# Kernel optimization log

Measured on AMD Instinct MI355X. Metric: run time of the kernel, lower is better.

The kernel has to match this reference:

```python
import jax, jax.numpy as jnp
from jax import lax
import numpy as np

B, N, E, U = 128, 1024, 300, 128
L = 512          # num_leaves per sample
NN = 2 * L - 1   # num_nodes per sample (binary tree)


def _hsig(x):
    # Keras hard_sigmoid: clip(0.2*x + 0.5, 0, 1)
    return jnp.clip(0.2 * x + 0.5, 0.0, 1.0)


def setup_inputs() -> dict:
    key = jax.random.key(0)
    ks = jax.random.split(key, 5)
    rng = np.random.default_rng(0)
    # children of node t are uniform in [0, t) -> valid bottom-up binary tree
    u = rng.random((B, N, 2))
    child = (u * np.arange(N)[None, :, None]).astype(np.int32)
    child[:, :L, :] = 0  # leaves have no children (never read)
    num_vecs = np.tile(np.array([[NN, L]], np.int32), (B, 1))
    return {
        "initial_state": jax.random.normal(ks[0], (B, N, E), jnp.float32),
        "translation_kernel": jax.random.normal(ks[1], (E, U), jnp.float32) * 0.05,
        "kernel": jax.random.normal(ks[2], (5 * U, U), jnp.float32) * 0.05,
        "recurrent_kernel": jax.random.normal(ks[3], (5 * U, 2 * U), jnp.float32) * 0.05,
        "bias": jnp.zeros((5 * U, 1), jnp.float32),
        "child_vecs": jnp.asarray(child),
        "num_vecs": jnp.asarray(num_vecs),
    }


def reference(initial_state, translation_kernel, kernel, recurrent_kernel, bias,
              child_vecs, num_vecs):
    b, n, _ = initial_state.shape
    units = kernel.shape[1]
    # leaf initial states: relu(x @ W_translate)  -> [B, N, U]
    x = jax.nn.relu(jnp.einsum('bne,eu->bnu', initial_state, translation_kernel))
    num_nodes = num_vecs[:, 0]
    num_leaves = num_vecs[:, 1]
    bvec = bias[:, 0][None, :]  # [1, 5U]

    def step(carry, t):
        H, C = carry  # [B, N, U] each
        ch = jnp.take(child_vecs, t, axis=1)                                   # [B, 2]
        h_ch = jnp.take_along_axis(H, ch[:, :, None], axis=1).reshape(b, 2 * units)
        c_ch = jnp.take_along_axis(C, ch[:, :, None], axis=1).reshape(b, 2 * units)
        xt = jnp.take(x, t, axis=1)                                            # [B, U]
        # z = kernel @ x^T + recurrent_kernel @ [h_l; h_r] + bias  (batched, [B, 5U])
        z = xt @ kernel.T + h_ch @ recurrent_kernel.T + bvec
        i = _hsig(z[:, :units])
        f = _hsig(z[:, units:3 * units])                                       # [B, 2U]
        o = _hsig(z[:, 3 * units:4 * units])
        g = jnp.tanh(z[:, 4 * units:])
        # faithful to original: reshape (flat_mem*f) as [U, 2] row-major, sum axis 1
        c_new = (c_ch * f).reshape(b, units, 2).sum(axis=-1) + i * g
        h_new = o * jnp.tanh(c_new)
        act = ((t >= num_leaves) & (t < num_nodes))[:, None]                   # [B, 1]
        h_upd = jnp.where(act, h_new, jnp.take(H, t, axis=1))
        c_upd = jnp.where(act, c_new, jnp.take(C, t, axis=1))
        H = lax.dynamic_update_slice(H, h_upd[:, None, :], (0, t, 0))
        C = lax.dynamic_update_slice(C, c_upd[:, None, :], (0, t, 0))
        return (H, C), None

    # leaves start with hidden = memory = translated vec; internal nodes overwritten in order
    (H, _), _ = lax.scan(step, (x, x), jnp.arange(n))
    valid = (jnp.arange(n)[None, :] < num_nodes[:, None])[..., None]
    return H * valid.astype(H.dtype)
```

## Files before the change

kernel.cpp:

```cpp
#include <hip/hip_runtime.h>
#include <hip/hip_bf16.h>

#define B_ 128
#define N_ 1024
#define E_ 300
#define U_ 128
#define M_ (B_ * N_)
#define Z_ (5 * U_)
#define LMAXT 40
#define LPAR 20

typedef __attribute__((ext_vector_type(8))) short bf16x8;
typedef __attribute__((ext_vector_type(4))) float f32x4;
typedef _Float16 f16x4 __attribute__((ext_vector_type(4)));
typedef _Float16 f16x8 __attribute__((ext_vector_type(8)));

__device__ __forceinline__ short f2bf(float f) {
  unsigned u = __builtin_bit_cast(unsigned, f);
  u = (u + 0x7fffu + ((u >> 16) & 1u)) >> 16;
  return (short)u;
}

__device__ __forceinline__ float hsig(float z) {
  float v = __builtin_fmaf(z, 0.2f, 0.5f);
  v = v < 0.f ? 0.f : v;
  v = v > 1.f ? 1.f : v;
  return v;
}

__device__ __forceinline__ float tanh_fast(float x) {
  float p = __expf(2.f * x);
  return 1.f - 2.f * __builtin_amdgcn_rcpf(p + 1.f);
}

__device__ __forceinline__ unsigned pk2(float a, float b) {
  return __builtin_bit_cast(unsigned, __builtin_amdgcn_cvt_pkrtz(a, b));
}

__device__ __forceinline__ f16x8 pack8(float4 a, float4 b) {
  uint4 u;
  u.x = pk2(a.x, a.y);
  u.y = pk2(a.z, a.w);
  u.z = pk2(b.x, b.y);
  u.w = pk2(b.z, b.w);
  return __builtin_bit_cast(f16x8, u);
}

__global__ __launch_bounds__(256) void prep(
    const float* __restrict__ Wr, const float* __restrict__ Wk,
    _Float16* __restrict__ W16, _Float16* __restrict__ Wk16) {
  const int idx = blockIdx.x * 256 + threadIdx.x;
  if (idx < 163840) {
    W16[idx] = (_Float16)Wr[idx];
  } else if (idx < 245760) {
    const int i = idx - 163840;
    Wk16[i] = (_Float16)Wk[i];
  }
}

__global__ __launch_bounds__(256) void x_gemm(
    const float* __restrict__ A, const float* __restrict__ W,
    float* __restrict__ H) {
  __shared__ __align__(16) short As[64][40];
  __shared__ __align__(16) short Ws[128][40];
  const int tid = threadIdx.x;
  const int m0 = blockIdx.x * 64;
  f32x4 acc[8] = {};
  const int lane = tid & 63, wv = tid >> 6;
  const int lr = lane & 15, lg = lane >> 4;

  for (int kc = 0; kc < 10; ++kc) {
    const int k0 = kc * 32;
    {
      const int row = tid >> 2, kk = (tid & 3) * 8;
      const float* src = A + (size_t)(m0 + row) * E_ + k0 + kk;
      bf16x8 v;
      if (k0 + 32 <= E_) {
#pragma unroll
        for (int i = 0; i < 8; ++i) v[i] = f2bf(src[i]);
      } else {
#pragma unroll
        for (int i = 0; i < 8; ++i)
          v[i] = (k0 + kk + i < E_) ? f2bf(src[i]) : (short)0;
      }
      *(bf16x8*)&As[row][kk] = v;
    }
#pragma unroll
    for (int s = 0; s < 2; ++s) {
      const int slot = tid + s * 256;
      const int n = slot & 127, kg = slot >> 7;
      bf16x8 v;
      if (k0 + 32 <= E_) {
#pragma unroll
        for (int i = 0; i < 8; ++i) v[i] = f2bf(W[(k0 + kg * 8 + i) * U_ + n]);
      } else {
#pragma unroll
        for (int i = 0; i < 8; ++i) {
          const int k = k0 + kg * 8 + i;
          v[i] = (k < E_) ? f2bf(W[k * U_ + n]) : (short)0;
        }
      }
      *(bf16x8*)&Ws[n][kg * 8] = v;
    }
    __syncthreads();
    bf16x8 a = *(const bf16x8*)&As[wv * 16 + lr][lg * 8];
#pragma unroll
    for (int nt = 0; nt < 8; ++nt) {
      bf16x8 b = *(const bf16x8*)&Ws[nt * 16 + lr][lg * 8];
      acc[nt] = __builtin_amdgcn_mfma_f32_16x16x32_bf16(a, b, acc[nt], 0, 0, 0);
    }
    __syncthreads();
  }
#pragma unroll
  for (int nt = 0; nt < 8; ++nt) {
#pragma unroll
    for (int r = 0; r < 4; ++r) {
      const int m = m0 + wv * 16 + lg * 4 + r;
      const int n = nt * 16 + lr;
      float v = acc[nt][r];
      v = v > 0.f ? v : 0.f;
      H[(size_t)m * U_ + n] = v;
    }
  }
}

__global__ __launch_bounds__(256) void xz_gemm(
    const float* __restrict__ X, const _Float16* __restrict__ Wk16,
    const float* __restrict__ bias, const int* __restrict__ nv,
    _Float16* __restrict__ XZ) {
  const int m0 = blockIdx.x * 64;
  {
    const int bb = m0 >> 10;
    const int t0 = m0 & (N_ - 1);
    const int nodes = nv[2 * bb], leaves = nv[2 * bb + 1];
    if (t0 + 64 <= leaves || t0 >= nodes) return;
  }
  __shared__ __align__(16) short As[64][40];
  __shared__ __align__(16) short Ws[128][40];
  __shared__ __align__(16) _Float16 xzls[64][136];
  const int tid = threadIdx.x;
  const int n0 = blockIdx.y * 128;
  f32x4 acc[8] = {};
  const int lane = tid & 63, wv = tid >> 6;
  const int lr = lane & 15, lg = lane >> 4;

  for (int kc = 0; kc < 4; ++kc) {
    const int k0 = kc * 32;
    {
      const int row = tid >> 2, kk = (tid & 3) * 8;
      const float* src = X + (size_t)(m0 + row) * U_ + k0 + kk;
      const float4 a0 = *(const float4*)src;
      const float4 a1 = *(const float4*)(src + 4);
      *(f16x8*)&As[row][kk] = pack8(a0, a1);
    }
#pragma unroll
    for (int s = 0; s < 2; ++s) {
      const int slot = tid + s * 256;
      const int n = slot >> 2, kk = (slot & 3) * 8;
      *(f16x8*)&Ws[n][kk] =
          *(const f16x8*)(Wk16 + (size_t)(n0 + n) * U_ + k0 + kk);
    }
    __syncthreads();
    f16x8 a = *(const f16x8*)&As[wv * 16 + lr][lg * 8];
#pragma unroll
    for (int nt = 0; nt < 8; ++nt) {
      f16x8 b = *(const f16x8*)&Ws[nt * 16 + lr][lg * 8];
      acc[nt] = __builtin_amdgcn_mfma_f32_16x16x32_f16(a, b, acc[nt], 0, 0, 0);
    }
    __syncthreads();
  }
#pragma unroll
  for (int nt = 0; nt < 8; ++nt) {
    const float bv = bias[n0 + nt * 16 + lr];
#pragma unroll
    for (int r = 0; r < 4; ++r)
      xzls[wv * 16 + lg * 4 + r][nt * 16 + lr] = (_Float16)(acc[nt][r] + bv);
  }
  __syncthreads();
  {
    const int row = tid >> 2, c0 = (tid & 3) * 32;
    _Float16* dst = XZ + (size_t)(m0 + row) * Z_ + n0 + c0;
#pragma unroll
    for (int s = 0; s < 4; ++s)
      *(f16x8*)(dst + 8 * s) = *(const f16x8*)&xzls[row][c0 + 8 * s];
  }
}

__global__ __launch_bounds__(512) void levelize(
    const int* __restrict__ child, const int* __restrict__ nv,
    unsigned char* __restrict__ lv, short* __restrict__ rank,
    int* __restrict__ cnt) {
  const int b = blockIdx.x;
  const int tid = threadIdx.x;
  int nodes = nv[2 * b];
  int leaves = nv[2 * b + 1];
  if (nodes > N_) nodes = N_;
  if (leaves < 0) leaves = 0;

  __shared__ short lvs[N_];
  __shared__ int chs[2 * N_];
  __shared__ int cnts[LMAXT];
  __shared__ int changed;

  for (int i = tid; i < N_; i += 512) lvs[i] = 0;
  for (int i = tid; i < 2 * N_; i += 512) chs[i] = child[(size_t)b * 2 * N_ + i];
  if (tid < LMAXT) cnts[tid] = 0;
  __syncthreads();

  int stable = 0;
  for (int s = 0; s < 64; ++s) {
    if (tid == 0) changed = 0;
    __syncthreads();
    int any = 0;
    for (int t = leaves + tid; t < nodes; t += 512) {
      const int c0 = chs[2 * t], c1 = chs[2 * t + 1];
      const int l0 = (c0 < t && c0 >= 0) ? lvs[c0] : 0;
      const int l1 = (c1 < t && c1 >= 0) ? lvs[c1] : 0;
      const int l = 1 + (l0 > l1 ? l0 : l1);
      if (l > (int)lvs[t]) { lvs[t] = (short)l; any = 1; }
    }
    if (any) changed = 1;
    __syncthreads();
    if (!changed) { stable = 1; break; }
  }
  if (!stable) {
    if (tid == 0) {
      for (int t = leaves; t < nodes; ++t) {
        const int c0 = chs[2 * t], c1 = chs[2 * t + 1];
        const int l0 = (c0 < t && c0 >= 0) ? lvs[c0] : 0;
        const int l1 = (c1 < t && c1 >= 0) ? lvs[c1] : 0;
        lvs[t] = (short)(1 + (l0 > l1 ? l0 : l1));
      }
    }
    __syncthreads();
  }

  for (int t = tid; t < nodes; t += 512) {
    int l = (t < leaves) ? 0 : (int)lvs[t];
    if (l > LMAXT - 1) l = LMAXT - 1;
    lv[b * N_ + t] = (unsigned char)l;
    if (t >= leaves && l < LMAXT - 1)
      rank[b * N_ + t] = (short)atomicAdd(&cnts[l], 1);
  }
  __syncthreads();
  if (tid == 0) {
    for (int t = leaves; t < nodes; ++t)
      if ((int)lvs[t] >= LMAXT - 1) rank[b * N_ + t] = (short)(cnts[LMAXT - 1]++);
  }
  __syncthreads();
  if (tid < LMAXT) cnt[tid * 128 + b] = cnts[tid];
}

__global__ __launch_bounds__(64) void offsets(
    const int* __restrict__ cnt, int* __restrict__ pos, int* __restrict__ goff) {
  const int l = threadIdx.x;
  __shared__ int tot[LMAXT];
  if (l < LMAXT) {
    int s = 0;
    for (int b = 0; b < 128; ++b) {
      pos[l * 128 + b] = s;
      s += cnt[l * 128 + b];
    }
    tot[l] = s;
  }
  __syncthreads();
  if (l == 0) {
    int g = 0;
    for (int i = 0; i < LMAXT; ++i) { goff[i] = g; g += tot[i]; }
    goff[LMAXT] = g;
  }
  __syncthreads();
  if (l < LMAXT) {
    const int g = goff[l];
    for (int b = 0; b < 128; ++b) pos[l * 128 + b] += g;
  }
}

__global__ __launch_bounds__(256) void scatter_zero(
    const int* __restrict__ nv, const unsigned char* __restrict__ lv,
    const short* __restrict__ rank, const int* __restrict__ pos,
    int* __restrict__ glist, float* __restrict__ H) {
  const int b = blockIdx.x;
  const int tid = threadIdx.x;
  int nodes = nv[2 * b];
  int leaves = nv[2 * b + 1];
  if (nodes > N_) nodes = N_;
  if (leaves < 0) leaves = 0;
  for (int t = leaves + tid; t < nodes; t += 256) {
    const int l = lv[b * N_ + t];
    glist[pos[l * 128 + b] + rank[b * N_ + t]] = (b << 10) | t;
  }
  const int total = (N_ - nodes) * U_;
  for (int idx = tid; idx < total; idx += 256)
    H[(size_t)b * N_ * U_ + nodes * U_ + idx] = 0.f;
}

struct ChunkLd {
  float4 a0, a1;
  float4 cv0, cv1;
  f16x4 xzi, xzo, xzg;
  f16x8 xzf;
  int nid, rem;
};

__device__ __forceinline__ ChunkLd load_chunk(
    int chunk, int nchunk, int base, int count, const int* __restrict__ glist,
    const int* __restrict__ child, const unsigned char* __restrict__ lv,
    const _Float16* __restrict__ XZ, const float* __restrict__ H,
    const float* __restrict__ C, int j, int s, int col, int u0, int mc) {
  ChunkLd r;
  const int cc = chunk < nchunk - 1 ? chunk : nchunk - 1;
  const int cb = base + cc * 16;
  int rem = count - cc * 16;
  if (rem > 16) rem = 16;
  r.rem = rem;

  const int nidj = glist[cb + (j < rem ? j : rem - 1)];
  const int bj = nidj >> 10, tj = nidj & 1023;
  const int chj = child[((size_t)bj << 11) + 2 * tj + (s >> 4)];
  const float* hsrc = H + (((size_t)(bj << 10) + chj) << 7) + ((s & 15) << 3);
  r.a0 = *(const float4*)hsrc;
  r.a1 = *(const float4*)(hsrc + 4);

  const int nidc = glist[cb + (col < rem ? col : rem - 1)];
  r.nid = nidc;
  const _Float16* xzr = XZ + (size_t)nidc * Z_;
  r.xzi = *(const f16x4*)(xzr + u0);
  r.xzf = *(const f16x8*)(xzr + 128 + mc);
  r.xzo = *(const f16x4*)(xzr + 384 + u0);
  r.xzg = *(const f16x4*)(xzr + 512 + u0);
  const int bc = nidc >> 10, tc = nidc & 1023;
  const int csel = child[((size_t)bc << 11) + 2 * tc + (mc >> 7)];
  const int crow = (bc << 10) | csel;
  const float* cbp =
      (lv[crow] == 0 ? H : C) + ((size_t)crow << 7) + (mc & 127);
  r.cv0 = ((const float4*)cbp)[0];
  r.cv1 = ((const float4*)cbp)[1];
  return r;
}

__global__ __launch_bounds__(512, 2) void level_gemm(
    int lvl, const _Float16* __restrict__ W16, const int* __restrict__ child,
    const unsigned char* __restrict__ lv, const int* __restrict__ goff,
    const int* __restrict__ glist, const _Float16* __restrict__ XZ,
    float* __restrict__ H, float* __restrict__ C) {
  const int base = goff[lvl];
  const int count = goff[lvl + 1] - base;
  if (count <= 0) return;
  const int nchunk = (count + 15) >> 4;
  if ((int)blockIdx.x >= nchunk) return;
  const int tid = threadIdx.x;
  const int lane = tid & 63, w = tid >> 6;
  const int col = lane & 15, hi = lane >> 4;
  const int u0 = 16 * w + 4 * hi;
  const int mc = 2 * u0;
  const int j = tid >> 5, s = tid & 31;

  f16x8 afrag[5][8];
  {
    const int rows[5] = {16 * w + col, 128 + 32 * w + 2 * col,
                         129 + 32 * w + 2 * col, 384 + 16 * w + col,
                         512 + 16 * w + col};
#pragma unroll
    for (int rt = 0; rt < 5; ++rt) {
      const _Float16* rs = W16 + (size_t)rows[rt] * 256 + 8 * hi;
#pragma unroll
      for (int kt = 0; kt < 8; ++kt) afrag[rt][kt] = *(const f16x8*)(rs + 32 * kt);
    }
  }

  __shared__ __align__(16) _Float16 hbuf[2][16][272];

  ChunkLd cur = load_chunk(blockIdx.x, nchunk, base, count, glist, child, lv,
                           XZ, H, C, j, s, col, u0, mc);
  int p = 0;
  for (int chunk = blockIdx.x; chunk < nchunk; chunk += gridDim.x) {
    uint4 hp;
    hp.x = pk2(cur.a0.x, cur.a0.y);
    hp.y = pk2(cur.a0.z, cur.a0.w);
    hp.z = pk2(cur.a1.x, cur.a1.y);
    hp.w = pk2(cur.a1.z, cur.a1.w);
    *(uint4*)&hbuf[p][j][(s >> 4) * 128 + (s & 15) * 8] = hp;

    ChunkLd nxt = load_chunk(chunk + gridDim.x < nchunk ? chunk + gridDim.x
                                                        : nchunk - 1,
                             nchunk, base, count, glist, child, lv, XZ, H, C,
                             j, s, col, u0, mc);

    asm volatile("s_waitcnt lgkmcnt(0)" ::: "memory");
    __builtin_amdgcn_sched_barrier(0);
    __builtin_amdgcn_s_barrier();
    __builtin_amdgcn_sched_barrier(0);

    f32x4 acc[5];
#pragma unroll
    for (int r = 0; r < 4; ++r) {
      acc[0][r] = (float)cur.xzi[r];
      acc[1][r] = (float)cur.xzf[2 * r];
      acc[2][r] = (float)cur.xzf[2 * r + 1];
      acc[3][r] = (float)cur.xzo[r];
      acc[4][r] = (float)cur.xzg[r];
    }
#pragma unroll
    for (int kt = 0; kt < 8; ++kt) {
      const f16x8 bf = *(const f16x8*)&hbuf[p][col][32 * kt + 8 * hi];
#pragma unroll
      for (int rt = 0; rt < 5; ++rt)
        acc[rt] = __builtin_amdgcn_mfma_f32_16x16x32_f16(afrag[rt][kt], bf,
                                                         acc[rt], 0, 0, 0);
    }

    const float ce[8] = {cur.cv0.x, cur.cv0.y, cur.cv0.z, cur.cv0.w,
                         cur.cv1.x, cur.cv1.y, cur.cv1.z, cur.cv1.w};
    f32x4 hn4, cn4;
#pragma unroll
    for (int r = 0; r < 4; ++r) {
      const float cn = ce[2 * r] * hsig(acc[1][r]) +
                       ce[2 * r + 1] * hsig(acc[2][r]) +
                       hsig(acc[0][r]) * tanh_fast(acc[4][r]);
      cn4[r] = cn;
      hn4[r] = hsig(acc[3][r]) * tanh_fast(cn);
    }
    if (col < cur.rem) {
      const size_t rowb = (size_t)cur.nid << 7;
      *(f32x4*)(H + rowb + u0) = hn4;
      *(f32x4*)(C + rowb + u0) = cn4;
    }
    cur = nxt;
    p ^= 1;
  }
}

__global__ __launch_bounds__(512, 2) void tail_scan(
    const _Float16* __restrict__ W16, const int* __restrict__ child,
    const unsigned char* __restrict__ lv, const int* __restrict__ nv,
    const int* __restrict__ pos, const int* __restrict__ cnt,
    const int* __restrict__ glist, const _Float16* __restrict__ XZ,
    float* __restrict__ H, float* __restrict__ C) {
  const int b = blockIdx.x;
  const int tid = threadIdx.x;
  const int lane = tid & 63, w = tid >> 6;
  const int col = lane & 15, hi = lane >> 4;
  const int u0 = 16 * w + 4 * hi;
  const int mc = 2 * u0;
  const int m4 = 4 * lane;

  f16x8 afrag[5][8];
  {
    const int rows[5] = {16 * w + col, 128 + 32 * w + 2 * col,
                         129 + 32 * w + 2 * col, 384 + 16 * w + col,
                         512 + 16 * w + col};
#pragma unroll
    for (int rt = 0; rt < 5; ++rt) {
      const _Float16* rs = W16 + (size_t)rows[rt] * 256 + 8 * hi;
#pragma unroll
      for (int kt = 0; kt < 8; ++kt) afrag[rt][kt] = *(const f16x8*)(rs + 32 * kt);
    }
  }

  __shared__ __align__(16) _Float16 hb1[256];
  const int* chb = child + (size_t)b * 2 * N_;
  const unsigned char* lvb = lv + (size_t)b * N_;
  float* Hb = H + (size_t)b * N_ * U_;
  float* Cb = C + (size_t)b * N_ * U_;
  const _Float16* xzb = XZ + (size_t)b * N_ * Z_;

  for (int l = LPAR; l < LMAXT; ++l) {
    const int p0 = pos[l * 128 + b];
    const int n = cnt[l * 128 + b];
    for (int i = 0; i < n; ++i) {
      const int t = glist[p0 + i] & 1023;
      if (tid < 64) {
        const int ch = chb[2 * t + (m4 >> 7)];
        const float4 hv = *(const float4*)(Hb + ((size_t)ch << 7) + (m4 & 127));
        uint2 hp;
        hp.x = pk2(hv.x, hv.y);
        hp.y = pk2(hv.z, hv.w);
        *(uint2*)&hb1[m4] = hp;
      }
      const int cs = chb[2 * t + (mc >> 7)];
      const float* cbp =
          (lvb[cs] == 0 ? Hb : Cb) + ((size_t)cs << 7) + (mc & 127);
      const float4 cv0 = ((const float4*)cbp)[0];
      const float4 cv1 = ((const float4*)cbp)[1];
      const _Float16* xzr = xzb + (size_t)t * Z_;
      const f16x4 xzi = *(const f16x4*)(xzr + u0);
      const f16x8 xzf = *(const f16x8*)(xzr + 128 + mc);
      const f16x4 xzo = *(const f16x4*)(xzr + 384 + u0);
      const f16x4 xzg = *(const f16x4*)(xzr + 512 + u0);
      __syncthreads();
      f32x4 acc[5];
#pragma unroll
      for (int r = 0; r < 4; ++r) {
        acc[0][r] = (float)xzi[r];
        acc[1][r] = (float)xzf[2 * r];
        acc[2][r] = (float)xzf[2 * r + 1];
        acc[3][r] = (float)xzo[r];
        acc[4][r] = (float)xzg[r];
      }
#pragma unroll
      for (int kt = 0; kt < 8; ++kt) {
        const f16x8 bf = *(const f16x8*)&hb1[32 * kt + 8 * hi];
#pragma unroll
        for (int rt = 0; rt < 5; ++rt)
          acc[rt] = __builtin_amdgcn_mfma_f32_16x16x32_f16(afrag[rt][kt], bf,
                                                           acc[rt], 0, 0, 0);
      }
      const float ce[8] = {cv0.x, cv0.y, cv0.z, cv0.w,
                           cv1.x, cv1.y, cv1.z, cv1.w};
      f32x4 hn4, cn4;
#pragma unroll
      for (int r = 0; r < 4; ++r) {
        const float cn = ce[2 * r] * hsig(acc[1][r]) +
                         ce[2 * r + 1] * hsig(acc[2][r]) +
                         hsig(acc[0][r]) * tanh_fast(acc[4][r]);
        cn4[r] = cn;
        hn4[r] = hsig(acc[3][r]) * tanh_fast(cn);
      }
      if (col == 0) {
        *(f32x4*)(Hb + ((size_t)t << 7) + u0) = hn4;
        *(f32x4*)(Cb + ((size_t)t << 7) + u0) = cn4;
      }
      __syncthreads();
    }
  }
}

extern "C" void kernel_launch(void* const* d_in, const int* in_sizes, int n_in,
                              void* d_out, int out_size, void* d_ws,
                              size_t ws_size, hipStream_t stream) {
  const float* state = (const float*)d_in[0];
  const float* tk    = (const float*)d_in[1];
  const float* Wk    = (const float*)d_in[2];
  const float* Wr    = (const float*)d_in[3];
  const float* bias  = (const float*)d_in[4];
  const int*   child = (const int*)d_in[5];
  const int*   nvp   = (const int*)d_in[6];
  float* H = (float*)d_out;

  char* wsb = (char*)d_ws;
  _Float16* W16   = (_Float16*)(wsb + 0x000000);
  _Float16* Wk16  = (_Float16*)(wsb + 0x050000);
  unsigned char* lv = (unsigned char*)(wsb + 0x078000);
  short* rank     = (short*)(wsb + 0x098000);
  int* cnt        = (int*)(wsb + 0x0D8000);
  int* pos        = (int*)(wsb + 0x0DD000);
  int* goff       = (int*)(wsb + 0x0E2000);
  int* glist      = (int*)(wsb + 0x0E3000);
  const size_t meta_sz = 2ull * 1024 * 1024;
  const size_t c_bytes = (size_t)M_ * U_ * sizeof(float);
  float* C = (float*)(wsb + meta_sz);
  _Float16* XZ = (_Float16*)(wsb + meta_sz + c_bytes);

  prep<<<960, 256, 0, stream>>>(Wr, Wk, W16, Wk16);
  x_gemm<<<M_ / 64, 256, 0, stream>>>(state, tk, H);
  xz_gemm<<<dim3(M_ / 64, 5), 256, 0, stream>>>(H, Wk16, bias, nvp, XZ);
  levelize<<<B_, 512, 0, stream>>>(child, nvp, lv, rank, cnt);
  offsets<<<1, 64, 0, stream>>>(cnt, pos, goff);
  scatter_zero<<<B_, 256, 0, stream>>>(nvp, lv, rank, pos, glist, H);
  static const int lg[LPAR] = {0,  512, 384, 256, 192, 128, 96, 64, 48, 32,
                               24, 20,  16,  16,  16,  16,  16, 16, 16, 16};
  for (int l = 1; l < LPAR; ++l)
    level_gemm<<<lg[l], 512, 0, stream>>>(l, W16, child, lv, goff, glist, XZ,
                                          H, C);
  tail_scan<<<B_, 512, 0, stream>>>(W16, child, lv, nvp, pos, cnt, glist, XZ,
                                    H, C);
}
```

Baseline: 427.4 us.

## Keep fp16 shadow copies of H and C for child gathers, pre-transpose translation weights

Adds fp16 mirror buffers H16/C16, initialized from the leaf states and written alongside the fp32 H for each internal node. The level and tail kernels now gather children from these halves, which removes the leaf/internal C select and halves gather bytes. The translation kernel is pre-transposed to bf16 once so x_gemm loads it with vector reads, and the level-parallel/tail-scan split moves from 20 levels to 12. The cost is an extra full-size conversion pass, extra fp16 stores, and memory cell values rounded to fp16, which may lose accuracy.

```diff
diff --git a/kernel.cpp b/kernel.cpp
--- a/kernel.cpp
+++ b/kernel.cpp
@@ -8,7 +8,7 @@
 #define M_ (B_ * N_)
 #define Z_ (5 * U_)
 #define LMAXT 40
-#define LPAR 20
+#define LPAR 12
 
 typedef __attribute__((ext_vector_type(8))) short bf16x8;
 typedef __attribute__((ext_vector_type(4))) float f32x4;
@@ -48,18 +48,23 @@
 
 __global__ __launch_bounds__(256) void prep(
     const float* __restrict__ Wr, const float* __restrict__ Wk,
-    _Float16* __restrict__ W16, _Float16* __restrict__ Wk16) {
+    const float* __restrict__ tk, _Float16* __restrict__ W16,
+    _Float16* __restrict__ Wk16, short* __restrict__ tkTb) {
   const int idx = blockIdx.x * 256 + threadIdx.x;
   if (idx < 163840) {
     W16[idx] = (_Float16)Wr[idx];
   } else if (idx < 245760) {
     const int i = idx - 163840;
     Wk16[i] = (_Float16)Wk[i];
+  } else if (idx < 286720) {
+    const int i = idx - 245760;
+    const int n = i / 320, k = i - n * 320;
+    tkTb[i] = (k < E_) ? f2bf(tk[k * U_ + n]) : (short)0;
   }
 }
 
 __global__ __launch_bounds__(256) void x_gemm(
-    const float* __restrict__ A, const float* __restrict__ W,
+    const float* __restrict__ A, const short* __restrict__ tkTb,
     float* __restrict__ H) {
   __shared__ __align__(16) short As[64][40];
   __shared__ __align__(16) short Ws[128][40];
@@ -89,18 +94,8 @@
     for (int s = 0; s < 2; ++s) {
       const int slot = tid + s * 256;
       const int n = slot & 127, kg = slot >> 7;
-      bf16x8 v;
-      if (k0 + 32 <= E_) {
-#pragma unroll
-        for (int i = 0; i < 8; ++i) v[i] = f2bf(W[(k0 + kg * 8 + i) * U_ + n]);
-      } else {
-#pragma unroll
-        for (int i = 0; i < 8; ++i) {
-          const int k = k0 + kg * 8 + i;
-          v[i] = (k < E_) ? f2bf(W[k * U_ + n]) : (short)0;
-        }
-      }
-      *(bf16x8*)&Ws[n][kg * 8] = v;
+      *(bf16x8*)&Ws[n][kg * 8] =
+          *(const bf16x8*)(tkTb + (size_t)n * 320 + k0 + kg * 8);
     }
     __syncthreads();
     bf16x8 a = *(const bf16x8*)&As[wv * 16 + lr][lg * 8];
@@ -121,6 +116,19 @@
       v = v > 0.f ? v : 0.f;
       H[(size_t)m * U_ + n] = v;
     }
+  }
+}
+
+__global__ __launch_bounds__(256) void h16c16(
+    const float* __restrict__ H, _Float16* __restrict__ H16,
+    _Float16* __restrict__ C16) {
+  const size_t i = ((size_t)blockIdx.x * 256 + threadIdx.x) * 8;
+  if (i < (size_t)M_ * U_) {
+    const float4 a0 = *(const float4*)(H + i);
+    const float4 a1 = *(const float4*)(H + i + 4);
+    const f16x8 v = pack8(a0, a1);
+    *(f16x8*)(H16 + i) = v;
+    *(f16x8*)(C16 + i) = v;
   }
 }
 
@@ -296,8 +304,8 @@
 }
 
 struct ChunkLd {
-  float4 a0, a1;
-  float4 cv0, cv1;
+  uint4 h16;
+  f16x8 cv16;
   f16x4 xzi, xzo, xzg;
   f16x8 xzf;
   int nid, rem;
@@ -305,9 +313,9 @@
 
 __device__ __forceinline__ ChunkLd load_chunk(
     int chunk, int nchunk, int base, int count, const int* __restrict__ glist,
-    const int* __restrict__ child, const unsigned char* __restrict__ lv,
-    const _Float16* __restrict__ XZ, const float* __restrict__ H,
-    const float* __restrict__ C, int j, int s, int col, int u0, int mc) {
+    const int* __restrict__ child, const _Float16* __restrict__ XZ,
+    const _Float16* __restrict__ H16, const _Float16* __restrict__ C16,
+    int j, int s, int col, int u0, int mc) {
   ChunkLd r;
   const int cc = chunk < nchunk - 1 ? chunk : nchunk - 1;
   const int cb = base + cc * 16;
@@ -318,9 +326,8 @@
   const int nidj = glist[cb + (j < rem ? j : rem - 1)];
   const int bj = nidj >> 10, tj = nidj & 1023;
   const int chj = child[((size_t)bj << 11) + 2 * tj + (s >> 4)];
-  const float* hsrc = H + (((size_t)(bj << 10) + chj) << 7) + ((s & 15) << 3);
-  r.a0 = *(const float4*)hsrc;
-  r.a1 = *(const float4*)(hsrc + 4);
+  r.h16 = *(const uint4*)(H16 + (((size_t)(bj << 10) + chj) << 7) +
+                          ((s & 15) << 3));
 
   const int nidc = glist[cb + (col < rem ? col : rem - 1)];
   r.nid = nidc;
@@ -332,18 +339,15 @@
   const int bc = nidc >> 10, tc = nidc & 1023;
   const int csel = child[((size_t)bc << 11) + 2 * tc + (mc >> 7)];
   const int crow = (bc << 10) | csel;
-  const float* cbp =
-      (lv[crow] == 0 ? H : C) + ((size_t)crow << 7) + (mc & 127);
-  r.cv0 = ((const float4*)cbp)[0];
-  r.cv1 = ((const float4*)cbp)[1];
+  r.cv16 = *(const f16x8*)(C16 + ((size_t)crow << 7) + (mc & 127));
   return r;
 }
 
 __global__ __launch_bounds__(512, 2) void level_gemm(
     int lvl, const _Float16* __restrict__ W16, const int* __restrict__ child,
-    const unsigned char* __restrict__ lv, const int* __restrict__ goff,
-    const int* __restrict__ glist, const _Float16* __restrict__ XZ,
-    float* __restrict__ H, float* __restrict__ C) {
+    const int* __restrict__ goff, const int* __restrict__ glist,
+    const _Float16* __restrict__ XZ, float* __restrict__ H,
+    _Float16* __restrict__ H16, _Float16* __restrict__ C16) {
   const int base = goff[lvl];
   const int count = goff[lvl + 1] - base;
   if (count <= 0) return;
@@ -371,20 +375,15 @@
 
   __shared__ __align__(16) _Float16 hbuf[2][16][272];
 
-  ChunkLd cur = load_chunk(blockIdx.x, nchunk, base, count, glist, child, lv,
-                           XZ, H, C, j, s, col, u0, mc);
+  ChunkLd cur = load_chunk(blockIdx.x, nchunk, base, count, glist, child, XZ,
+                           H16, C16, j, s, col, u0, mc);
   int p = 0;
   for (int chunk = blockIdx.x; chunk < nchunk; chunk += gridDim.x) {
-    uint4 hp;
-    hp.x = pk2(cur.a0.x, cur.a0.y);
-    hp.y = pk2(cur.a0.z, cur.a0.w);
-    hp.z = pk2(cur.a1.x, cur.a1.y);
-    hp.w = pk2(cur.a1.z, cur.a1.w);
-    *(uint4*)&hbuf[p][j][(s >> 4) * 128 + (s & 15) * 8] = hp;
+    *(uint4*)&hbuf[p][j][(s >> 4) * 128 + (s & 15) * 8] = cur.h16;
 
     ChunkLd nxt = load_chunk(chunk + gridDim.x < nchunk ? chunk + gridDim.x
                                                         : nchunk - 1,
-                             nchunk, base, count, glist, child, lv, XZ, H, C,
+                             nchunk, base, count, glist, child, XZ, H16, C16,
                              j, s, col, u0, mc);
 
     asm volatile("s_waitcnt lgkmcnt(0)" ::: "memory");
@@ -410,13 +409,11 @@
                                                          acc[rt], 0, 0, 0);
     }
 
-    const float ce[8] = {cur.cv0.x, cur.cv0.y, cur.cv0.z, cur.cv0.w,
-                         cur.cv1.x, cur.cv1.y, cur.cv1.z, cur.cv1.w};
     f32x4 hn4, cn4;
 #pragma unroll
     for (int r = 0; r < 4; ++r) {
-      const float cn = ce[2 * r] * hsig(acc[1][r]) +
-                       ce[2 * r + 1] * hsig(acc[2][r]) +
+      const float cn = (float)cur.cv16[2 * r] * hsig(acc[1][r]) +
+                       (float)cur.cv16[2 * r + 1] * hsig(acc[2][r]) +
                        hsig(acc[0][r]) * tanh_fast(acc[4][r]);
       cn4[r] = cn;
       hn4[r] = hsig(acc[3][r]) * tanh_fast(cn);
@@ -424,7 +421,13 @@
     if (col < cur.rem) {
       const size_t rowb = (size_t)cur.nid << 7;
       *(f32x4*)(H + rowb + u0) = hn4;
-      *(f32x4*)(C + rowb + u0) = cn4;
+      uint2 hp16, cp16;
+      hp16.x = pk2(hn4[0], hn4[1]);
+      hp16.y = pk2(hn4[2], hn4[3]);
+      cp16.x = pk2(cn4[0], cn4[1]);
+      cp16.y = pk2(cn4[2], cn4[3]);
+      *(uint2*)(H16 + rowb + u0) = hp16;
+      *(uint2*)(C16 + rowb + u0) = cp16;
     }
     cur = nxt;
     p ^= 1;
@@ -433,10 +436,10 @@
 
 __global__ __launch_bounds__(512, 2) void tail_scan(
     const _Float16* __restrict__ W16, const int* __restrict__ child,
-    const unsigned char* __restrict__ lv, const int* __restrict__ nv,
-    const int* __restrict__ pos, const int* __restrict__ cnt,
-    const int* __restrict__ glist, const _Float16* __restrict__ XZ,
-    float* __restrict__ H, float* __restrict__ C) {
+    const int* __restrict__ nv, const int* __restrict__ pos,
+    const int* __restrict__ cnt, const int* __restrict__ glist,
+    const _Float16* __restrict__ XZ, float* __restrict__ H,
+    _Float16* __restrict__ H16, _Float16* __restrict__ C16) {
   const int b = blockIdx.x;
   const int tid = threadIdx.x;
   const int lane = tid & 63, w = tid >> 6;
@@ -460,9 +463,9 @@
 
   __shared__ __align__(16) _Float16 hb1[256];
   const int* chb = child + (size_t)b * 2 * N_;
-  const unsigned char* lvb = lv + (size_t)b * N_;
   float* Hb = H + (size_t)b * N_ * U_;
-  float* Cb = C + (size_t)b * N_ * U_;
+  _Float16* Hb16 = H16 + (size_t)b * N_ * U_;
+  _Float16* Cb16 = C16 + (size_t)b * N_ * U_;
   const _Float16* xzb = XZ + (size_t)b * N_ * Z_;
 
   for (int l = LPAR; l < LMAXT; ++l) {
@@ -472,17 +475,12 @@
       const int t = glist[p0 + i] & 1023;
       if (tid < 64) {
         const int ch = chb[2 * t + (m4 >> 7)];
-        const float4 hv = *(const float4*)(Hb + ((size_t)ch << 7) + (m4 & 127));
-        uint2 hp;
-        hp.x = pk2(hv.x, hv.y);
-        hp.y = pk2(hv.z, hv.w);
-        *(uint2*)&hb1[m4] = hp;
+        *(uint2*)&hb1[m4] =
+            *(const uint2*)(Hb16 + ((size_t)ch << 7) + (m4 & 127));
       }
       const int cs = chb[2 * t + (mc >> 7)];
-      const float* cbp =
-          (lvb[cs] == 0 ? Hb : Cb) + ((size_t)cs << 7) + (mc & 127);
-      const float4 cv0 = ((const float4*)cbp)[0];
-      const float4 cv1 = ((const float4*)cbp)[1];
+      const f16x8 cv16 =
+          *(const f16x8*)(Cb16 + ((size_t)cs << 7) + (mc & 127));
       const _Float16* xzr = xzb + (size_t)t * Z_;
       const f16x4 xzi = *(const f16x4*)(xzr + u0);
       const f16x8 xzf = *(const f16x8*)(xzr + 128 + mc);
@@ -506,20 +504,24 @@
           acc[rt] = __builtin_amdgcn_mfma_f32_16x16x32_f16(afrag[rt][kt], bf,
                                                            acc[rt], 0, 0, 0);
       }
-      const float ce[8] = {cv0.x, cv0.y, cv0.z, cv0.w,
-                           cv1.x, cv1.y, cv1.z, cv1.w};
       f32x4 hn4, cn4;
 #pragma unroll
       for (int r = 0; r < 4; ++r) {
-        const float cn = ce[2 * r] * hsig(acc[1][r]) +
-                         ce[2 * r + 1] * hsig(acc[2][r]) +
+        const float cn = (float)cv16[2 * r] * hsig(acc[1][r]) +
+                         (float)cv16[2 * r + 1] * hsig(acc[2][r]) +
                          hsig(acc[0][r]) * tanh_fast(acc[4][r]);
         cn4[r] = cn;
         hn4[r] = hsig(acc[3][r]) * tanh_fast(cn);
       }
       if (col == 0) {
         *(f32x4*)(Hb + ((size_t)t << 7) + u0) = hn4;
-        *(f32x4*)(Cb + ((size_t)t << 7) + u0) = cn4;
+        uint2 hp16, cp16;
+        hp16.x = pk2(hn4[0], hn4[1]);
+        hp16.y = pk2(hn4[2], hn4[3]);
+        cp16.x = pk2(cn4[0], cn4[1]);
+        cp16.y = pk2(cn4[2], cn4[3]);
+        *(uint2*)(Hb16 + ((size_t)t << 7) + u0) = hp16;
+        *(uint2*)(Cb16 + ((size_t)t << 7) + u0) = cp16;
       }
       __syncthreads();
     }
@@ -541,28 +543,31 @@
   char* wsb = (char*)d_ws;
   _Float16* W16   = (_Float16*)(wsb + 0x000000);
   _Float16* Wk16  = (_Float16*)(wsb + 0x050000);
-  unsigned char* lv = (unsigned char*)(wsb + 0x078000);
-  short* rank     = (short*)(wsb + 0x098000);
-  int* cnt        = (int*)(wsb + 0x0D8000);
-  int* pos        = (int*)(wsb + 0x0DD000);
-  int* goff       = (int*)(wsb + 0x0E2000);
-  int* glist      = (int*)(wsb + 0x0E3000);
+  short* tkTb     = (short*)(wsb + 0x078000);
+  unsigned char* lv = (unsigned char*)(wsb + 0x08C000);
+  short* rank     = (short*)(wsb + 0x0AC000);
+  int* cnt        = (int*)(wsb + 0x0EC000);
+  int* pos        = (int*)(wsb + 0x0F1000);
+  int* goff       = (int*)(wsb + 0x0F6000);
+  int* glist      = (int*)(wsb + 0x0F7000);
   const size_t meta_sz = 2ull * 1024 * 1024;
-  const size_t c_bytes = (size_t)M_ * U_ * sizeof(float);
-  float* C = (float*)(wsb + meta_sz);
-  _Float16* XZ = (_Float16*)(wsb + meta_sz + c_bytes);
-
-  prep<<<960, 256, 0, stream>>>(Wr, Wk, W16, Wk16);
-  x_gemm<<<M_ / 64, 256, 0, stream>>>(state, tk, H);
+  const size_t h16_bytes = (size_t)M_ * U_ * 2;
+  _Float16* H16 = (_Float16*)(wsb + meta_sz);
+  _Float16* C16 = (_Float16*)(wsb + meta_sz + h16_bytes);
+  _Float16* XZ  = (_Float16*)(wsb + meta_sz + 2 * h16_bytes);
+
+  prep<<<1120, 256, 0, stream>>>(Wr, Wk, tk, W16, Wk16, tkTb);
+  x_gemm<<<M_ / 64, 256, 0, stream>>>(state, tkTb, H);
+  h16c16<<<(M_ * U_ / 8 + 255) / 256, 256, 0, stream>>>(H, H16, C16);
   xz_gemm<<<dim3(M_ / 64, 5), 256, 0, stream>>>(H, Wk16, bias, nvp, XZ);
   levelize<<<B_, 512, 0, stream>>>(child, nvp, lv, rank, cnt);
   offsets<<<1, 64, 0, stream>>>(cnt, pos, goff);
   scatter_zero<<<B_, 256, 0, stream>>>(nvp, lv, rank, pos, glist, H);
-  static const int lg[LPAR] = {0,  512, 384, 256, 192, 128, 96, 64, 48, 32,
-                               24, 20,  16,  16,  16,  16,  16, 16, 16, 16};
+  static const int lg[LPAR] = {0,  512, 384, 256, 192, 128,
+                               96, 64,  48,  32,  24,  20};
   for (int l = 1; l < LPAR; ++l)
-    level_gemm<<<lg[l], 512, 0, stream>>>(l, W16, child, lv, goff, glist, XZ,
-                                          H, C);
-  tail_scan<<<B_, 512, 0, stream>>>(W16, child, lv, nvp, pos, cnt, glist, XZ,
-                                    H, C);
-}
+    level_gemm<<<lg[l], 512, 0, stream>>>(l, W16, child, goff, glist, XZ, H,
+                                          H16, C16);
+  tail_scan<<<B_, 512, 0, stream>>>(W16, child, nvp, pos, cnt, glist, XZ, H,
+                                    H16, C16);
+}
```

Result: no change. 431.2 us (+0.9%).
